# Kernel tuning notes

Measured on AMD Instinct MI355X. Metric: run time of the kernel, lower is better.

## Reference

```python
import jax, jax.numpy as jnp
import numpy as np

D_MODEL = 1024
NUM_HEADS = 16
HEAD_DIM = D_MODEL // NUM_HEADS


def setup_inputs() -> dict:
    key = jax.random.key(0)
    ks = jax.random.split(key, 12)
    B, S, D = 4, 2048, D_MODEL
    s = 1.0 / np.sqrt(D)
    return {
        "query": jax.random.normal(ks[0], (B, S, D), jnp.float32),
        "key": jax.random.normal(ks[1], (B, S, D), jnp.float32),
        "value": jax.random.normal(ks[2], (B, S, D), jnp.float32),
        "Wq": jax.random.normal(ks[3], (D, D), jnp.float32) * s,
        "bq": jax.random.normal(ks[4], (D,), jnp.float32) * 0.02,
        "Wk": jax.random.normal(ks[5], (D, D), jnp.float32) * s,
        "bk": jax.random.normal(ks[6], (D,), jnp.float32) * 0.02,
        "Wv": jax.random.normal(ks[7], (D, D), jnp.float32) * s,
        "bv": jax.random.normal(ks[8], (D,), jnp.float32) * 0.02,
        "Wo": jax.random.normal(ks[9], (D, D), jnp.float32) * s,
        "bo": jax.random.normal(ks[10], (D,), jnp.float32) * 0.02,
    }


def _split_heads(x):
    B, S, D = x.shape
    return x.reshape(B, S, NUM_HEADS, HEAD_DIM).transpose(0, 2, 1, 3)  # [B,H,S,hd]


def reference(query, key, value, Wq, bq, Wk, bk, Wv, bv, Wo, bo):
    q = _split_heads(query @ Wq + bq)
    k = _split_heads(key @ Wk + bk)
    v = _split_heads(value @ Wv + bv)
    # NOTE: original scales by 1/sqrt(d_model), not 1/sqrt(head_dim)
    scale = 1.0 / np.sqrt(D_MODEL).astype(np.float32)
    scores = jnp.einsum('bhqd,bhkd->bhqk', q, k) * scale  # [B,H,S,S]
    attn = jax.nn.softmax(scores, axis=-1)
    out = jnp.einsum('bhqk,bhkd->bhqd', attn, v)  # [B,H,S,hd]
    B, H, S, hd = out.shape
    out = out.transpose(0, 2, 1, 3).reshape(B, S, D_MODEL)
    out = out @ Wo + bo
    return out, attn
```

## Files before the change

### kernel.cpp

```cpp
#include <hip/hip_runtime.h>
#include <hip/hip_bf16.h>

typedef __bf16 bf16;
typedef __bf16 bf16x8 __attribute__((ext_vector_type(8)));
typedef __bf16 bf16x4 __attribute__((ext_vector_type(4)));
typedef __bf16 bf16x2 __attribute__((ext_vector_type(2)));
typedef float  f32x4  __attribute__((ext_vector_type(4)));
typedef float  f32x16 __attribute__((ext_vector_type(16)));
typedef unsigned int u32;

#define MFMA(A, B, C)   __builtin_amdgcn_mfma_f32_16x16x32_bf16((A), (B), (C), 0, 0, 0)
#define MFMA32(A, B, C) __builtin_amdgcn_mfma_f32_32x32x16_bf16((A), (B), (C), 0, 0, 0)

static constexpr int BATCH = 4, S = 2048, D = 1024, NH = 16, HD = 64;
static constexpr int M = BATCH * S;
static constexpr float KL = 0.045084220027780106f;

__device__ __forceinline__ void gload16(const void* g, void* l) {
  __builtin_amdgcn_global_load_lds(
      (const __attribute__((address_space(1))) void*)g,
      (__attribute__((address_space(3))) void*)l, 16, 0, 0);
}

__device__ __forceinline__ float fexp2(float x) {
#if __has_builtin(__builtin_amdgcn_exp2f)
  return __builtin_amdgcn_exp2f(x);
#else
  return exp2f(x);
#endif
}

__device__ __forceinline__ u32 pack2(float a, float b) {
  union { bf16x2 h; u32 u; } c;
  c.h = (bf16x2){(bf16)a, (bf16)b};
  return c.u;
}

union U4 { u32 w[4]; bf16x8 v; };

#define WAITV_BAR(n)                                                     \
  asm volatile("s_waitcnt vmcnt(" #n ") lgkmcnt(0)" ::: "memory");       \
  __builtin_amdgcn_s_barrier();                                          \
  __builtin_amdgcn_sched_barrier(0);

#define FENCE_BAR                                                        \
  asm volatile("s_waitcnt lgkmcnt(0)" ::: "memory");                     \
  __builtin_amdgcn_s_barrier();                                          \
  __builtin_amdgcn_sched_barrier(0);

__global__ __launch_bounds__(256) void convert_all(
    const float* __restrict__ X0, const float* __restrict__ X1,
    const float* __restrict__ X2,
    const float* __restrict__ W0, const float* __restrict__ W1,
    const float* __restrict__ W2, const float* __restrict__ W3,
    bf16* __restrict__ Xb, bf16* __restrict__ WtAll)
{
  int blk = blockIdx.x;
  int tid = threadIdx.x;
  if (blk < 6144) {
    int t = blk >> 11;
    int bx = blk & 2047;
    const float* X = t == 0 ? X0 : t == 1 ? X1 : X2;
    bf16* Yp = Xb + (size_t)t * M * D;
    int idx = bx * 256 + tid;
#pragma unroll
    for (int i = 0; i < 4; ++i) {
      size_t j = (size_t)idx + (size_t)i * 524288;
      float4 v = reinterpret_cast<const float4*>(X)[j];
      bf16x4 o; o[0] = (bf16)v.x; o[1] = (bf16)v.y; o[2] = (bf16)v.z; o[3] = (bf16)v.w;
      reinterpret_cast<bf16x4*>(Yp)[j] = o;
    }
  } else {
    int wb = blk - 6144;
    int wy = wb >> 8;
    int bx = wb & 255;
    const float* W = wy == 0 ? W0 : wy == 1 ? W1 : wy == 2 ? W2 : W3;
    bf16* dst = WtAll + (size_t)wy * (D * D);
    int k0 = (bx >> 4) * 64, n0 = (bx & 15) * 64;
    __shared__ __align__(16) bf16 T[64][72];
#pragma unroll
    for (int i = 0; i < 4; ++i) {
      int c = tid + i * 256, r = c >> 4, seg = c & 15;
      float4 v = *reinterpret_cast<const float4*>(W + (size_t)(k0 + r) * D + n0 + seg * 4);
      T[seg * 4 + 0][r] = (bf16)v.x; T[seg * 4 + 1][r] = (bf16)v.y;
      T[seg * 4 + 2][r] = (bf16)v.z; T[seg * 4 + 3][r] = (bf16)v.w;
    }
    __syncthreads();
#pragma unroll
    for (int i = 0; i < 2; ++i) {
      int c = tid + i * 256, r = c >> 3, seg = c & 7;
      *reinterpret_cast<bf16x8*>(dst + (size_t)(n0 + r) * D + k0 + seg * 8) =
          *reinterpret_cast<const bf16x8*>(&T[r][seg * 8]);
    }
  }
}

__global__ __launch_bounds__(256) void qkv_gemm(
    const bf16* __restrict__ Xb, const bf16* __restrict__ WtAll,
    const float* __restrict__ bq, const float* __restrict__ bk, const float* __restrict__ bv,
    bf16* __restrict__ Qb, bf16* __restrict__ Kb, bf16* __restrict__ Vtb)
{
  int v = blockIdx.y;
  const bf16*  X    = Xb + (size_t)v * M * D;
  const bf16*  Wt   = WtAll + (size_t)v * (D * D);
  const float* bias = v == 0 ? bq : v == 1 ? bk : bv;

  int x = blockIdx.x;
  int swz = (x & 7) * 64 + (x >> 3);
  int mt = swz >> 3, nt = swz & 7;
  int m0 = mt * 128, n0 = nt * 128;
  int tid = threadIdx.x, lane = tid & 63, w = tid >> 6;
  int wm = (w >> 1) * 64, wn = (w & 1) * 64;
  int lr = lane & 15, lg = lane >> 4;

  __shared__ __align__(16) unsigned char smem[34816];
  auto As = reinterpret_cast<bf16(*)[128][32]>(smem);
  auto Bs = reinterpret_cast<bf16(*)[128][32]>(smem + 16384);

  f32x4 acc[4][4] = {};

  int srow = w * 32 + (lane >> 2);
  int scol = (lane & 3) * 8;

  auto stage = [&](int buf, int ks) {
    const bf16* ga = X + (size_t)(m0 + srow) * D + ks * 32 + scol;
    bf16* la = &As[buf][w * 32][0];
    gload16(ga, la);
    gload16(ga + 16 * D, la + 16 * 32);
    const bf16* gb = Wt + (size_t)(n0 + srow) * D + ks * 32 + scol;
    bf16* lb = &Bs[buf][w * 32][0];
    gload16(gb, lb);
    gload16(gb + 16 * D, lb + 16 * 32);
  };

  stage(0, 0);
  for (int ks = 0; ks < 32; ++ks) {
    __syncthreads();
    if (ks < 31) stage((ks + 1) & 1, ks + 1);
    int buf = ks & 1;
    bf16x8 af[4], bfr[4];
#pragma unroll
    for (int i = 0; i < 4; ++i)
      af[i] = *reinterpret_cast<const bf16x8*>(&As[buf][wm + i * 16 + lr][8 * lg]);
#pragma unroll
    for (int j = 0; j < 4; ++j)
      bfr[j] = *reinterpret_cast<const bf16x8*>(&Bs[buf][wn + j * 16 + lr][8 * lg]);
#pragma unroll
    for (int i = 0; i < 4; ++i)
#pragma unroll
      for (int j = 0; j < 4; ++j)
        acc[i][j] = MFMA(af[i], bfr[j], acc[i][j]);
  }
  __syncthreads();

  if (v < 2) {
    bf16* Out = v == 0 ? Qb : Kb;
    float qs = v == 0 ? KL : 1.0f;
    auto Es = reinterpret_cast<bf16(*)[128]>(smem);
#pragma unroll
    for (int i = 0; i < 4; ++i)
#pragma unroll
      for (int j = 0; j < 4; ++j) {
        int n = wn + j * 16 + lr;
        float bias_n = bias[n0 + n];
#pragma unroll
        for (int r = 0; r < 4; ++r)
          Es[wm + i * 16 + 4 * lg + r][n] = (bf16)((acc[i][j][r] + bias_n) * qs);
      }
    __syncthreads();
#pragma unroll
    for (int i = 0; i < 8; ++i) {
      int c = tid + i * 256, r = c >> 4, seg = c & 15;
      int mg = m0 + r, b = mg >> 11, s = mg & 2047;
      int ng = n0 + seg * 8, h = ng >> 6, d = ng & 63;
      *reinterpret_cast<bf16x8*>(Out + (((size_t)(b * NH + h)) * S + s) * HD + d) =
          *reinterpret_cast<const bf16x8*>(&Es[r][seg * 8]);
    }
  } else {
    auto Es = reinterpret_cast<bf16(*)[136]>(smem);
#pragma unroll
    for (int i = 0; i < 4; ++i)
#pragma unroll
      for (int j = 0; j < 4; ++j) {
        int n = wn + j * 16 + lr;
        float bias_n = bias[n0 + n];
        bf16x4 t;
#pragma unroll
        for (int r = 0; r < 4; ++r) t[r] = (bf16)(acc[i][j][r] + bias_n);
        *reinterpret_cast<bf16x4*>(&Es[n][wm + i * 16 + 4 * lg]) = t;
      }
    __syncthreads();
#pragma unroll
    for (int i = 0; i < 8; ++i) {
      int c = tid + i * 256, r = c >> 4, seg = c & 15;
      int ng = n0 + r, h = ng >> 6, d = ng & 63;
      int mg = m0 + seg * 8, b = mg >> 11, s = mg & 2047;
      *reinterpret_cast<bf16x8*>(Vtb + (((size_t)(b * NH + h)) * HD + d) * S + s) =
          *reinterpret_cast<const bf16x8*>(&Es[r][seg * 8]);
    }
  }
}

__global__ __launch_bounds__(256) void attn_kernel(
    const bf16* __restrict__ Qb, const bf16* __restrict__ Kb, const bf16* __restrict__ Vtb,
    float* __restrict__ attn_out, bf16* __restrict__ ctx)
{
  int xx = blockIdx.x;
  int xcd = xx & 7, r8 = xx >> 3;
  int bh = xcd + 8 * (r8 >> 5);
  int qb = r8 & 31;
  int tid = threadIdx.x, lane = tid & 63, w = tid >> 6;
  int q32 = lane & 31, hi = lane >> 5;
  int qh = w & 1, kh = w >> 1;

  __shared__ __align__(16) bf16 Ks[2][64][64];
  __shared__ __align__(16) bf16 Vs[2][64][64];
  __shared__ __align__(16) float Ps[64][68];
  __shared__ float sums[2][64];

  int q_row = qb * 64 + qh * 32 + q32;
  const bf16* Qrow = Qb + ((size_t)bh * S + q_row) * HD;
  bf16x8 qreg[4];
#pragma unroll
  for (int c = 0; c < 4; ++c)
    qreg[c] = *reinterpret_cast<const bf16x8*>(Qrow + c * 16 + 8 * hi);

  auto stageK = [&](int buf, int kc) {
    const bf16* base = Kb + ((size_t)bh * S + kc * 64) * HD;
#pragma unroll
    for (int i = 0; i < 2; ++i) {
      int c = i * 256 + tid, row = c >> 3, j = c & 7;
      gload16(base + row * HD + 8 * (j ^ (row & 7)),
              reinterpret_cast<bf16*>(&Ks[buf][0][0]) + c * 8);
    }
  };
  auto stageV = [&](int buf, int kc) {
    const bf16* base = Vtb + (size_t)bh * HD * S + kc * 64;
#pragma unroll
    for (int i = 0; i < 2; ++i) {
      int c = i * 256 + tid, row = c >> 3, j = c & 7;
      gload16(base + (size_t)row * S + 8 * (j ^ (row & 7)),
              reinterpret_cast<bf16*>(&Vs[buf][0][0]) + c * 8);
    }
  };

  int krow = kh * 32 + q32, ks7 = krow & 7;

  float xs[4] = {0.f, 0.f, 0.f, 0.f};
  stageK(0, 0);
  for (int kc = 0; kc < 32; ++kc) {
    if (kc < 31) {
      stageK((kc + 1) & 1, kc + 1);
      WAITV_BAR(2)
    } else {
      WAITV_BAR(0)
    }
    int buf = kc & 1;
    f32x16 sa = {};
#pragma unroll
    for (int c = 0; c < 4; ++c) {
      bf16x8 kf = *reinterpret_cast<const bf16x8*>(&Ks[buf][krow][8 * ((2 * c + hi) ^ ks7)]);
      sa = MFMA32(kf, qreg[c], sa);
    }
#pragma unroll
    for (int r = 0; r < 16; ++r) xs[r & 3] += fexp2(sa[r]);
    FENCE_BAR
  }
  float lrun = (xs[0] + xs[1]) + (xs[2] + xs[3]);
  lrun += __shfl_xor(lrun, 32);
  if (hi == 0) sums[kh][qh * 32 + q32] = lrun;
  __syncthreads();
  float lg2l = __log2f(sums[0][qh * 32 + q32] + sums[1][qh * 32 + q32]);

  f32x16 oaccA = {}, oaccB = {};
  float* ablk = attn_out + ((size_t)bh * S + qb * 64) * S;

  auto computeB = [&](int buf) {
    f32x16 sa = {};
#pragma unroll
    for (int c = 0; c < 4; ++c) {
      bf16x8 kf = *reinterpret_cast<const bf16x8*>(&Ks[buf][krow][8 * ((2 * c + hi) ^ ks7)]);
      sa = MFMA32(kf, qreg[c], sa);
    }
    u32 pku[8];
#pragma unroll
    for (int rq = 0; rq < 4; ++rq) {
      f32x4 pv;
#pragma unroll
      for (int j = 0; j < 4; ++j) pv[j] = fexp2(sa[rq * 4 + j] - lg2l);
      *reinterpret_cast<f32x4*>(&Ps[qh * 32 + q32][kh * 32 + 8 * rq + 4 * hi]) = pv;
      pku[rq * 2 + 0] = pack2(pv[0], pv[1]);
      pku[rq * 2 + 1] = pack2(pv[2], pv[3]);
    }
#pragma unroll
    for (int c2 = 0; c2 < 2; ++c2) {
      u32 myw0 = hi ? pku[4 * c2 + 2] : pku[4 * c2 + 0];
      u32 myw1 = hi ? pku[4 * c2 + 3] : pku[4 * c2 + 1];
      u32 sdw0 = hi ? pku[4 * c2 + 0] : pku[4 * c2 + 2];
      u32 sdw1 = hi ? pku[4 * c2 + 1] : pku[4 * c2 + 3];
      u32 r0 = __shfl_xor(sdw0, 32);
      u32 r1 = __shfl_xor(sdw1, 32);
      U4 f;
      f.w[0] = hi ? r0 : myw0;
      f.w[1] = hi ? r1 : myw1;
      f.w[2] = hi ? myw0 : r0;
      f.w[3] = hi ? myw1 : r1;
      {
        int vrow = q32, vs7 = vrow & 7;
        bf16x8 vf = *reinterpret_cast<const bf16x8*>(
            &Vs[buf][vrow][8 * ((4 * kh + 2 * c2 + hi) ^ vs7)]);
        oaccA = MFMA32(f.v, vf, oaccA);
      }
      {
        int vrow = 32 + q32, vs7 = vrow & 7;
        bf16x8 vf = *reinterpret_cast<const bf16x8*>(
            &Vs[buf][vrow][8 * ((4 * kh + 2 * c2 + hi) ^ vs7)]);
        oaccB = MFMA32(f.v, vf, oaccB);
      }
    }
  };

  int r16 = tid >> 4, c16 = (tid & 15) * 4;
  auto storeP = [&](int kc) {
#pragma unroll
    for (int s = 0; s < 4; ++s) {
      int row = s * 16 + r16;
      __builtin_nontemporal_store(
          *reinterpret_cast<const f32x4*>(&Ps[row][c16]),
          reinterpret_cast<f32x4*>(ablk + (size_t)row * S + kc * 64 + c16));
    }
  };

  stageK(0, 0); stageV(0, 0);
  stageK(1, 1); stageV(1, 1);
  WAITV_BAR(4)
  computeB(0);
  FENCE_BAR
  storeP(0);

  for (int kc = 1; kc < 32; ++kc) {
    if (kc < 31) {
      stageK((kc + 1) & 1, kc + 1);
      stageV((kc + 1) & 1, kc + 1);
      WAITV_BAR(8)
    } else {
      WAITV_BAR(4)
    }
    computeB(kc & 1);
    FENCE_BAR
    storeP(kc);
  }

  float* fbuf = reinterpret_cast<float*>(&Ks[0][0][0]);
  __syncthreads();
  if (kh == 1) {
#pragma unroll
    for (int reg = 0; reg < 16; ++reg) {
      int qloc = (reg & 3) + 8 * (reg >> 2) + 4 * hi;
      fbuf[(qh * 32 + qloc) * 64 + q32]      = oaccA[reg];
      fbuf[(qh * 32 + qloc) * 64 + 32 + q32] = oaccB[reg];
    }
  }
  __syncthreads();
  bf16* cs = reinterpret_cast<bf16*>(&Vs[0][0][0]);
  if (kh == 0) {
#pragma unroll
    for (int reg = 0; reg < 16; ++reg) {
      int qloc = (reg & 3) + 8 * (reg >> 2) + 4 * hi;
      cs[(qh * 32 + qloc) * 72 + q32] =
          (bf16)(oaccA[reg] + fbuf[(qh * 32 + qloc) * 64 + q32]);
      cs[(qh * 32 + qloc) * 72 + 32 + q32] =
          (bf16)(oaccB[reg] + fbuf[(qh * 32 + qloc) * 64 + 32 + q32]);
    }
  }
  __syncthreads();
  {
    int b = bh >> 4, h = bh & 15;
    int row = tid >> 2, cseg = (tid & 3) * 16;
    bf16* cp = ctx + ((size_t)b * S + qb * 64 + row) * D + h * HD + cseg;
    *reinterpret_cast<bf16x8*>(cp) =
        *reinterpret_cast<const bf16x8*>(&cs[row * 72 + cseg]);
    *reinterpret_cast<bf16x8*>(cp + 8) =
        *reinterpret_cast<const bf16x8*>(&cs[row * 72 + cseg + 8]);
  }
}

__global__ __launch_bounds__(256) void out_gemm(
    const bf16* __restrict__ ctx, const bf16* __restrict__ Wto,
    const float* __restrict__ bo, float* __restrict__ Out)
{
  int x = blockIdx.x;
  int swz = (x & 7) * 64 + (x >> 3);
  int mt = swz >> 3, nt = swz & 7;
  int m0 = mt * 128, n0 = nt * 128;
  int tid = threadIdx.x, lane = tid & 63, w = tid >> 6;
  int wm = (w >> 1) * 64, wn = (w & 1) * 64;
  int lr = lane & 15, lg = lane >> 4;

  __shared__ __align__(16) bf16 As[2][128][32];
  __shared__ __align__(16) bf16 Bs[2][128][32];

  f32x4 acc[4][4] = {};

  int srow = w * 32 + (lane >> 2);
  int scol = (lane & 3) * 8;

  auto stage = [&](int buf, int ks) {
    const bf16* ga = ctx + (size_t)(m0 + srow) * D + ks * 32 + scol;
    bf16* la = &As[buf][w * 32][0];
    gload16(ga, la);
    gload16(ga + 16 * D, la + 16 * 32);
    const bf16* gb = Wto + (size_t)(n0 + srow) * D + ks * 32 + scol;
    bf16* lb = &Bs[buf][w * 32][0];
    gload16(gb, lb);
    gload16(gb + 16 * D, lb + 16 * 32);
  };

  stage(0, 0);
  for (int ks = 0; ks < 32; ++ks) {
    __syncthreads();
    if (ks < 31) stage((ks + 1) & 1, ks + 1);
    int buf = ks & 1;
    bf16x8 af[4], bfr[4];
#pragma unroll
    for (int i = 0; i < 4; ++i)
      af[i] = *reinterpret_cast<const bf16x8*>(&As[buf][wm + i * 16 + lr][8 * lg]);
#pragma unroll
    for (int j = 0; j < 4; ++j)
      bfr[j] = *reinterpret_cast<const bf16x8*>(&Bs[buf][wn + j * 16 + lr][8 * lg]);
#pragma unroll
    for (int i = 0; i < 4; ++i)
#pragma unroll
      for (int j = 0; j < 4; ++j)
        acc[i][j] = MFMA(af[i], bfr[j], acc[i][j]);
  }

#pragma unroll
  for (int i = 0; i < 4; ++i)
#pragma unroll
    for (int j = 0; j < 4; ++j) {
      int n = n0 + wn + j * 16 + lr;
      float bias_n = bo[n];
#pragma unroll
      for (int r = 0; r < 4; ++r)
        Out[(size_t)(m0 + wm + i * 16 + 4 * lg + r) * D + n] = acc[i][j][r] + bias_n;
    }
}

extern "C" void kernel_launch(void* const* d_in, const int* in_sizes, int n_in,
                              void* d_out, int out_size, void* d_ws, size_t ws_size,
                              hipStream_t stream)
{
  const float* query = (const float*)d_in[0];
  const float* key   = (const float*)d_in[1];
  const float* value = (const float*)d_in[2];
  const float* Wq = (const float*)d_in[3]; const float* bq = (const float*)d_in[4];
  const float* Wk = (const float*)d_in[5]; const float* bk = (const float*)d_in[6];
  const float* Wv = (const float*)d_in[7]; const float* bv = (const float*)d_in[8];
  const float* Wo = (const float*)d_in[9]; const float* bo = (const float*)d_in[10];

  float* out  = (float*)d_out;
  float* attn = out + (size_t)M * D;

  char* ws = (char*)d_ws;
  const size_t MiB = 1048576;
  bf16* WtAll = (bf16*)ws;
  bf16* Xb    = (bf16*)(ws + 8 * MiB);
  bf16* Qb    = (bf16*)(ws + 56 * MiB);
  bf16* Kb    = (bf16*)(ws + 72 * MiB);
  bf16* Vtb   = (bf16*)(ws + 88 * MiB);
  bf16* ctx   = Xb;

  convert_all<<<dim3(7168), 256, 0, stream>>>(query, key, value,
                                              Wq, Wk, Wv, Wo, Xb, WtAll);
  qkv_gemm<<<dim3(512, 3), 256, 0, stream>>>(Xb, WtAll, bq, bk, bv, Qb, Kb, Vtb);
  attn_kernel<<<dim3(2048), 256, 0, stream>>>(Qb, Kb, Vtb, attn, ctx);
  out_gemm<<<dim3(512), 256, 0, stream>>>(ctx, WtAll + (size_t)3 * D * D, bo, out);
}
```

Before: 381.6 us.

## Process 128 query rows per attention block with 512 threads

Each attention workgroup now covers 128 query rows using 8 waves instead of 64 rows with 4 waves. Every staged K/V tile in LDS is shared by twice as many queries, which halves K/V global traffic and the number of staging loads per thread. The probability buffer and the row-sum array grow to match. The context write-back is split into two halves, and the cross-wave reduction buffer is reused from Ps. In exchange, per-block LDS use rises, which may limit how many blocks fit on a CU. The large attention-probability store, which likely dominates runtime, is unchanged.

```diff
diff --git a/kernel.cpp b/kernel.cpp
--- a/kernel.cpp
+++ b/kernel.cpp
@@ -201,24 +201,24 @@
   }
 }
 
-__global__ __launch_bounds__(256) void attn_kernel(
+__global__ __launch_bounds__(512, 4) void attn_kernel(
     const bf16* __restrict__ Qb, const bf16* __restrict__ Kb, const bf16* __restrict__ Vtb,
     float* __restrict__ attn_out, bf16* __restrict__ ctx)
 {
   int xx = blockIdx.x;
   int xcd = xx & 7, r8 = xx >> 3;
-  int bh = xcd + 8 * (r8 >> 5);
-  int qb = r8 & 31;
+  int bh = xcd + 8 * (r8 >> 4);
+  int qp = r8 & 15;
   int tid = threadIdx.x, lane = tid & 63, w = tid >> 6;
   int q32 = lane & 31, hi = lane >> 5;
-  int qh = w & 1, kh = w >> 1;
+  int qh = w & 3, kh = w >> 2;
 
   __shared__ __align__(16) bf16 Ks[2][64][64];
   __shared__ __align__(16) bf16 Vs[2][64][64];
-  __shared__ __align__(16) float Ps[64][68];
-  __shared__ float sums[2][64];
-
-  int q_row = qb * 64 + qh * 32 + q32;
+  __shared__ __align__(16) float Ps[128][68];
+  __shared__ float sums[2][128];
+
+  int q_row = qp * 128 + qh * 32 + q32;
   const bf16* Qrow = Qb + ((size_t)bh * S + q_row) * HD;
   bf16x8 qreg[4];
 #pragma unroll
@@ -227,21 +227,15 @@
 
   auto stageK = [&](int buf, int kc) {
     const bf16* base = Kb + ((size_t)bh * S + kc * 64) * HD;
-#pragma unroll
-    for (int i = 0; i < 2; ++i) {
-      int c = i * 256 + tid, row = c >> 3, j = c & 7;
-      gload16(base + row * HD + 8 * (j ^ (row & 7)),
-              reinterpret_cast<bf16*>(&Ks[buf][0][0]) + c * 8);
-    }
+    int row = tid >> 3, j = tid & 7;
+    gload16(base + row * HD + 8 * (j ^ (row & 7)),
+            reinterpret_cast<bf16*>(&Ks[buf][0][0]) + tid * 8);
   };
   auto stageV = [&](int buf, int kc) {
     const bf16* base = Vtb + (size_t)bh * HD * S + kc * 64;
-#pragma unroll
-    for (int i = 0; i < 2; ++i) {
-      int c = i * 256 + tid, row = c >> 3, j = c & 7;
-      gload16(base + (size_t)row * S + 8 * (j ^ (row & 7)),
-              reinterpret_cast<bf16*>(&Vs[buf][0][0]) + c * 8);
-    }
+    int row = tid >> 3, j = tid & 7;
+    gload16(base + (size_t)row * S + 8 * (j ^ (row & 7)),
+            reinterpret_cast<bf16*>(&Vs[buf][0][0]) + tid * 8);
   };
 
   int krow = kh * 32 + q32, ks7 = krow & 7;
@@ -251,7 +245,7 @@
   for (int kc = 0; kc < 32; ++kc) {
     if (kc < 31) {
       stageK((kc + 1) & 1, kc + 1);
-      WAITV_BAR(2)
+      WAITV_BAR(1)
     } else {
       WAITV_BAR(0)
     }
@@ -273,7 +267,7 @@
   float lg2l = __log2f(sums[0][qh * 32 + q32] + sums[1][qh * 32 + q32]);
 
   f32x16 oaccA = {}, oaccB = {};
-  float* ablk = attn_out + ((size_t)bh * S + qb * 64) * S;
+  float* ablk = attn_out + ((size_t)bh * S + qp * 128) * S;
 
   auto computeB = [&](int buf) {
     f32x16 sa = {};
@@ -324,7 +318,7 @@
   auto storeP = [&](int kc) {
 #pragma unroll
     for (int s = 0; s < 4; ++s) {
-      int row = s * 16 + r16;
+      int row = s * 32 + r16;
       __builtin_nontemporal_store(
           *reinterpret_cast<const f32x4*>(&Ps[row][c16]),
           reinterpret_cast<f32x4*>(ablk + (size_t)row * S + kc * 64 + c16));
@@ -333,7 +327,7 @@
 
   stageK(0, 0); stageV(0, 0);
   stageK(1, 1); stageV(1, 1);
-  WAITV_BAR(4)
+  WAITV_BAR(2)
   computeB(0);
   FENCE_BAR
   storeP(0);
@@ -342,7 +336,7 @@
     if (kc < 31) {
       stageK((kc + 1) & 1, kc + 1);
       stageV((kc + 1) & 1, kc + 1);
-      WAITV_BAR(8)
+      WAITV_BAR(6)
     } else {
       WAITV_BAR(4)
     }
@@ -351,7 +345,7 @@
     storeP(kc);
   }
 
-  float* fbuf = reinterpret_cast<float*>(&Ks[0][0][0]);
+  float* fbuf = &Ps[0][0];
   __syncthreads();
   if (kh == 1) {
 #pragma unroll
@@ -363,25 +357,30 @@
   }
   __syncthreads();
   bf16* cs = reinterpret_cast<bf16*>(&Vs[0][0][0]);
-  if (kh == 0) {
-#pragma unroll
-    for (int reg = 0; reg < 16; ++reg) {
-      int qloc = (reg & 3) + 8 * (reg >> 2) + 4 * hi;
-      cs[(qh * 32 + qloc) * 72 + q32] =
-          (bf16)(oaccA[reg] + fbuf[(qh * 32 + qloc) * 64 + q32]);
-      cs[(qh * 32 + qloc) * 72 + 32 + q32] =
-          (bf16)(oaccB[reg] + fbuf[(qh * 32 + qloc) * 64 + 32 + q32]);
-    }
-  }
-  __syncthreads();
-  {
-    int b = bh >> 4, h = bh & 15;
-    int row = tid >> 2, cseg = (tid & 3) * 16;
-    bf16* cp = ctx + ((size_t)b * S + qb * 64 + row) * D + h * HD + cseg;
-    *reinterpret_cast<bf16x8*>(cp) =
-        *reinterpret_cast<const bf16x8*>(&cs[row * 72 + cseg]);
-    *reinterpret_cast<bf16x8*>(cp + 8) =
-        *reinterpret_cast<const bf16x8*>(&cs[row * 72 + cseg + 8]);
+  int b = bh >> 4, h = bh & 15;
+#pragma unroll
+  for (int half = 0; half < 2; ++half) {
+    if (kh == 0 && (qh >> 1) == half) {
+      int qr32 = (qh & 1) * 32;
+#pragma unroll
+      for (int reg = 0; reg < 16; ++reg) {
+        int qloc = (reg & 3) + 8 * (reg >> 2) + 4 * hi;
+        int gq = qh * 32 + qloc;
+        cs[(qr32 + qloc) * 72 + q32] =
+            (bf16)(oaccA[reg] + fbuf[gq * 64 + q32]);
+        cs[(qr32 + qloc) * 72 + 32 + q32] =
+            (bf16)(oaccB[reg] + fbuf[gq * 64 + 32 + q32]);
+      }
+    }
+    __syncthreads();
+    {
+      int row = tid >> 3, cseg = (tid & 7) * 8;
+      bf16* cp = ctx + ((size_t)b * S + qp * 128 + half * 64 + row) * D
+                 + h * HD + cseg;
+      *reinterpret_cast<bf16x8*>(cp) =
+          *reinterpret_cast<const bf16x8*>(&cs[row * 72 + cseg]);
+    }
+    __syncthreads();
   }
 }
 
@@ -474,6 +473,6 @@
   convert_all<<<dim3(7168), 256, 0, stream>>>(query, key, value,
                                               Wq, Wk, Wv, Wo, Xb, WtAll);
   qkv_gemm<<<dim3(512, 3), 256, 0, stream>>>(Xb, WtAll, bq, bk, bv, Qb, Kb, Vtb);
-  attn_kernel<<<dim3(2048), 256, 0, stream>>>(Qb, Kb, Vtb, attn, ctx);
+  attn_kernel<<<dim3(1024), 512, 0, stream>>>(Qb, Kb, Vtb, attn, ctx);
   out_gemm<<<dim3(512), 256, 0, stream>>>(ctx, WtAll + (size_t)3 * D * D, bo, out);
 }
```

After: 376.2 us. No clear change (-1.4%).
